# Optimization experiments

Hardware: AMD Instinct MI355X
Metric: run time of the kernel (lower is better)

The kernel has to match this reference:

```python
import jax, jax.numpy as jnp
import numpy as np

SIGMA_SPATIAL = 1.0
SIGMA_BILATERAL = 0.25
RADIUS = 1
PATCH = 2 * RADIUS + 1  # 3


def _spatial_kernel():
    x, y = np.mgrid[-RADIUS:RADIUS + 1, -RADIUS:RADIUS + 1]
    w1 = np.exp(-(x ** 2 + y ** 2) / (2.0 * SIGMA_SPATIAL ** 2))
    return jnp.asarray(w1.reshape(-1), dtype=jnp.float32)  # [PATCH*PATCH]


def _extract_patches(x):
    # x: [B,H,W,C] -> [B,H,W,PATCH*PATCH,C] via reflect-padded shifted slices
    B, H, W, C = x.shape
    xp = jnp.pad(x, ((0, 0), (RADIUS, RADIUS), (RADIUS, RADIUS), (0, 0)), mode='reflect')
    return jnp.stack(
        [xp[:, dy:dy + H, dx:dx + W, :] for dy in range(PATCH) for dx in range(PATCH)],
        axis=3,
    )


def setup_inputs() -> dict:
    key = jax.random.key(0)
    k1, k2 = jax.random.split(key)
    src = jax.random.uniform(k1, (2, 512, 512, 21), dtype=jnp.float32)
    im = jax.random.uniform(k2, (2, 512, 512, 3), dtype=jnp.float32)
    return {"src": src, "im": im}


def reference(src, im):
    w1 = _spatial_kernel()  # [9]
    im_patches = _extract_patches(im)                      # [B,H,W,9,Ci]
    diff2 = jnp.sum((im_patches - im[:, :, :, None, :]) ** 2, axis=-1)  # [B,H,W,9]
    w = jnp.exp(-diff2 / (2.0 * SIGMA_BILATERAL ** 2)) * w1            # [B,H,W,9]
    src_patches = _extract_patches(src)                    # [B,H,W,9,Cs]
    num = jnp.sum(src_patches * w[..., None], axis=3)      # [B,H,W,Cs]
    den = jnp.sum(w, axis=3, keepdims=True)                # [B,H,W,1]
    return num / den
```

## Files before the change

### kernel.cpp

```cpp
#include <hip/hip_runtime.h>

#define BATCH 2
#define H 512
#define W 512
#define CS 21
#define CI 3
#define P 128
#define R 8
#define TPB 384
#define GROWS (R + 2)
#define GSL (P + 2)
#define GSZ (GROWS * GSL * CI)

typedef float f32x4 __attribute__((ext_vector_type(4)));

__device__ __forceinline__ void fma4(float4& a, const float4 v, const float w) {
    a.x = fmaf(v.x, w, a.x);
    a.y = fmaf(v.y, w, a.y);
    a.z = fmaf(v.z, w, a.z);
    a.w = fmaf(v.w, w, a.w);
}

__device__ __forceinline__ void nt_store4(float* p, const float4 v) {
    __builtin_nontemporal_store(*(const f32x4*)&v, (f32x4*)p);
}

#define LOAD3(dst, rr, om, oc, op)                              \
    (dst)[0] = *(const float4*)(srow[rr] + (om));               \
    (dst)[1] = *(const float4*)(srow[rr] + (oc));               \
    (dst)[2] = *(const float4*)(srow[rr] + (op));

#define VA_I(r) ((r) < 6 ? (r) : 5)
#define VB_I(r) ((r) < 6 ? 0 : (r) - 6)
#define VR(va, vb, r, k) ((r) < 6 ? (va)[VA_I(r)][(k)] : (vb)[VB_I(r)][(k)])

#define COMPUTE8(va, vb, px, oc)                                             \
    {                                                                        \
        _Pragma("unroll")                                                    \
        for (int j = 0; j < R; ++j) {                                        \
            const float* wd = &s_w[((j << 7) + (px)) * 12];                  \
            float4 wA = *(const float4*)(wd + 0);                            \
            float4 wB = *(const float4*)(wd + 4);                            \
            float  w8 = wd[8];                                               \
            float4 acc = {0.f, 0.f, 0.f, 0.f};                               \
            fma4(acc, VR(va, vb, j + 0, 0), wA.x);                           \
            fma4(acc, VR(va, vb, j + 0, 1), wA.y);                           \
            fma4(acc, VR(va, vb, j + 0, 2), wA.z);                           \
            fma4(acc, VR(va, vb, j + 1, 0), wA.w);                           \
            fma4(acc, VR(va, vb, j + 1, 1), wB.x);                           \
            fma4(acc, VR(va, vb, j + 1, 2), wB.y);                           \
            fma4(acc, VR(va, vb, j + 2, 0), wB.z);                           \
            fma4(acc, VR(va, vb, j + 2, 1), wB.w);                           \
            fma4(acc, VR(va, vb, j + 2, 2), w8);                             \
            nt_store4(ob + (size_t)j * rs + (oc), acc);                      \
        }                                                                    \
    }

__global__ __launch_bounds__(TPB, 3) void jbu_kernel(
    const float* __restrict__ src, const float* __restrict__ im,
    float* __restrict__ out)
{
    __shared__ float s_g[GSZ];
    __shared__ __align__(16) float s_w[R * P * 12];

    const int t = threadIdx.x;

    const int f      = blockIdx.x;
    const int xcd    = f & 7;
    const int g      = f >> 3;
    const int rowgrp = (xcd << 3) | (g & 7);
    const int rem    = g >> 3;
    const int x0     = (rem & 3) << 7;
    const int b      = rem >> 2;
    const int y0     = rowgrp << 3;

    const size_t rs = (size_t)W * CS;
    const float* sb = src + (size_t)b * H * rs;
    const float* srow[GROWS];
    #pragma unroll
    for (int rr = 0; rr < GROWS; ++rr) {
        int v = y0 - 1 + rr;
        int tyr = (v < 0) ? 1 : ((v >= H) ? 2 * H - 2 - v : v);
        srow[rr] = sb + (size_t)tyr * rs + (size_t)x0 * CS;
    }

    const int px0   = t / 6;
    const int q0    = t - px0 * 6;
    const int coff0 = (q0 == 5) ? 17 : (q0 << 2);
    const int x_    = x0 + px0;
    const int xm_   = (x_ == 0)     ? 1     : x_ - 1;
    const int xp_   = (x_ == W - 1) ? W - 2 : x_ + 1;
    const int om0   = (xm_ - x0) * CS + coff0;
    const int oc0   = px0 * CS + coff0;
    const int op0   = (xp_ - x0) * CS + coff0;

    float4 va0[6][3];
    #pragma unroll
    for (int rr = 0; rr < 6; ++rr) { LOAD3(va0[rr], rr, om0, oc0, op0) }

    const float* imb = im + (size_t)b * (H * W * CI);
    for (int i = t; i < GSZ; i += TPB) {
        int rr   = i / (GSL * CI);
        int remi = i - rr * (GSL * CI);
        int slot = remi / CI;
        int ch   = remi - slot * CI;
        int gx   = x0 + slot - 1;
        gx = (gx < 0) ? 1 : ((gx >= W) ? W - 2 : gx);
        int vv = y0 - 1 + rr;
        int tyr = (vv < 0) ? 1 : ((vv >= H) ? 2 * H - 2 - vv : vv);
        const float* gsrc = imb + ((size_t)tyr * W + gx) * CI + ch;
        __builtin_amdgcn_global_load_lds(
            (const __attribute__((address_space(1))) void*)gsrc,
            (__attribute__((address_space(3))) void*)(s_g + i), 4, 0, 0);
    }
    __syncthreads();

    const int item1 = TPB + t;
    const int px1   = item1 / 6;
    const int q1    = item1 - px1 * 6;
    const int coff1 = (q1 == 5) ? 17 : (q1 << 2);
    const int x1    = x0 + px1;
    const int xm1   = (x1 == 0)     ? 1     : x1 - 1;
    const int xp1   = (x1 == W - 1) ? W - 2 : x1 + 1;
    const int om1   = (xm1 - x0) * CS + coff1;
    const int oc1   = px1 * CS + coff1;
    const int op1   = (xp1 - x0) * CS + coff1;

    float4 va1[6][3];
    #pragma unroll
    for (int rr = 0; rr < 4; ++rr) { LOAD3(va1[rr], rr, om1, oc1, op1) }

    {
        const float w1k[9] = {0.36787944f, 0.60653066f, 0.36787944f,
                              0.60653066f, 1.0f,        0.60653066f,
                              0.36787944f, 0.60653066f, 0.36787944f};
        #pragma unroll
        for (int ii = 0; ii < 3; ++ii) {
            int idx = ii * TPB + t;
            if (idx < R * P) {
                int r   = idx >> 7;
                int px  = idx & (P - 1);
                int cb  = ((r + 1) * GSL + px + 1) * CI;
                float c0 = s_g[cb + 0], c1 = s_g[cb + 1], c2 = s_g[cb + 2];
                float wv[9];
                float den = 0.f;
                #pragma unroll
                for (int k = 0; k < 9; ++k) {
                    int dy = k / 3, dx = k % 3;
                    int ib = ((r + dy) * GSL + px + dx) * CI;
                    float d0 = s_g[ib + 0] - c0;
                    float d1 = s_g[ib + 1] - c1;
                    float d2 = s_g[ib + 2] - c2;
                    float w = __expf(-8.0f * (d0 * d0 + d1 * d1 + d2 * d2)) * w1k[k];
                    wv[k] = w;
                    den += w;
                }
                float inv = 1.0f / den;
                float* wd = &s_w[idx * 12];
                *(float4*)(wd + 0) = make_float4(wv[0] * inv, wv[1] * inv, wv[2] * inv, wv[3] * inv);
                *(float4*)(wd + 4) = make_float4(wv[4] * inv, wv[5] * inv, wv[6] * inv, wv[7] * inv);
                wd[8] = wv[8] * inv;
            }
        }
    }
    __syncthreads();

    float* ob = out + ((size_t)(b * H + y0)) * rs + (size_t)x0 * CS;

    {
        float4 vb0[4][3];
        #pragma unroll
        for (int rr = 0; rr < 4; ++rr) { LOAD3(vb0[rr], rr + 6, om0, oc0, op0) }
        COMPUTE8(va0, vb0, px0, oc0)
    }

    {
        LOAD3(va1[4], 4, om1, oc1, op1)
        LOAD3(va1[5], 5, om1, oc1, op1)
        float4 vb1[4][3];
        #pragma unroll
        for (int rr = 0; rr < 4; ++rr) { LOAD3(vb1[rr], rr + 6, om1, oc1, op1) }
        COMPUTE8(va1, vb1, px1, oc1)
    }
}

extern "C" void kernel_launch(void* const* d_in, const int* in_sizes, int n_in,
                              void* d_out, int out_size, void* d_ws, size_t ws_size,
                              hipStream_t stream) {
    const float* src = (const float*)d_in[0];
    const float* im  = (const float*)d_in[1];
    float* out = (float*)d_out;
    dim3 grid((W / P) * (H / R) * BATCH, 1, 1);
    jbu_kernel<<<grid, TPB, 0, stream>>>(src, im, out);
}
```

Before: 106.3 us.

## Shrink tiles to 32 pixels, alias guide and weight LDS, one item per thread

Narrows each block's tile from 128 to 32 columns and halves threads per block, so every thread now handles one pixel/channel-group item instead of two. The guide-image buffer and the weight table now share one LDS array: weights are computed into registers, a barrier follows, and then they are written over the guide data. Grid size grows fourfold and LDS per block drops, which should allow more resident blocks and lower register pressure. In exchange, the 2-pixel halo is a larger fraction of each tile, so more redundant src and guide loads, and there is an extra barrier.

```diff
diff --git a/kernel.cpp b/kernel.cpp
--- a/kernel.cpp
+++ b/kernel.cpp
@@ -5,12 +5,14 @@
 #define W 512
 #define CS 21
 #define CI 3
-#define P 128
+#define P 32
 #define R 8
-#define TPB 384
+#define TPB 192
 #define GROWS (R + 2)
 #define GSL (P + 2)
 #define GSZ (GROWS * GSL * CI)
+#define NSETS (R * P)
+#define SWF (NSETS * 12)
 
 typedef float f32x4 __attribute__((ext_vector_type(4)));
 
@@ -38,7 +40,7 @@
     {                                                                        \
         _Pragma("unroll")                                                    \
         for (int j = 0; j < R; ++j) {                                        \
-            const float* wd = &s_w[((j << 7) + (px)) * 12];                  \
+            const float* wd = &s_u[((j * P) + (px)) * 12];                   \
             float4 wA = *(const float4*)(wd + 0);                            \
             float4 wB = *(const float4*)(wd + 4);                            \
             float  w8 = wd[8];                                               \
@@ -60,8 +62,7 @@
     const float* __restrict__ src, const float* __restrict__ im,
     float* __restrict__ out)
 {
-    __shared__ float s_g[GSZ];
-    __shared__ __align__(16) float s_w[R * P * 12];
+    __shared__ __align__(16) float s_u[SWF];
 
     const int t = threadIdx.x;
 
@@ -70,8 +71,8 @@
     const int g      = f >> 3;
     const int rowgrp = (xcd << 3) | (g & 7);
     const int rem    = g >> 3;
-    const int x0     = (rem & 3) << 7;
-    const int b      = rem >> 2;
+    const int x0     = (rem & 15) << 5;
+    const int b      = rem >> 4;
     const int y0     = rowgrp << 3;
 
     const size_t rs = (size_t)W * CS;
@@ -96,92 +97,83 @@
 
     float4 va0[6][3];
     #pragma unroll
-    for (int rr = 0; rr < 6; ++rr) { LOAD3(va0[rr], rr, om0, oc0, op0) }
+    for (int rr = 0; rr < 4; ++rr) { LOAD3(va0[rr], rr, om0, oc0, op0) }
 
     const float* imb = im + (size_t)b * (H * W * CI);
-    for (int i = t; i < GSZ; i += TPB) {
-        int rr   = i / (GSL * CI);
-        int remi = i - rr * (GSL * CI);
-        int slot = remi / CI;
-        int ch   = remi - slot * CI;
-        int gx   = x0 + slot - 1;
-        gx = (gx < 0) ? 1 : ((gx >= W) ? W - 2 : gx);
-        int vv = y0 - 1 + rr;
-        int tyr = (vv < 0) ? 1 : ((vv >= H) ? 2 * H - 2 - vv : vv);
-        const float* gsrc = imb + ((size_t)tyr * W + gx) * CI + ch;
-        __builtin_amdgcn_global_load_lds(
-            (const __attribute__((address_space(1))) void*)gsrc,
-            (__attribute__((address_space(3))) void*)(s_g + i), 4, 0, 0);
+    #pragma unroll
+    for (int ii = 0; ii < (GSZ + TPB - 1) / TPB; ++ii) {
+        int i = ii * TPB + t;
+        if (i < GSZ) {
+            int rr   = i / (GSL * CI);
+            int remi = i - rr * (GSL * CI);
+            int slot = remi / CI;
+            int ch   = remi - slot * CI;
+            int gx   = x0 + slot - 1;
+            gx = (gx < 0) ? 1 : ((gx >= W) ? W - 2 : gx);
+            int vv = y0 - 1 + rr;
+            int tyr = (vv < 0) ? 1 : ((vv >= H) ? 2 * H - 2 - vv : vv);
+            const float* gsrc = imb + ((size_t)tyr * W + gx) * CI + ch;
+            __builtin_amdgcn_global_load_lds(
+                (const __attribute__((address_space(1))) void*)gsrc,
+                (__attribute__((address_space(3))) void*)(s_u + i), 4, 0, 0);
+        }
     }
     __syncthreads();
 
-    const int item1 = TPB + t;
-    const int px1   = item1 / 6;
-    const int q1    = item1 - px1 * 6;
-    const int coff1 = (q1 == 5) ? 17 : (q1 << 2);
-    const int x1    = x0 + px1;
-    const int xm1   = (x1 == 0)     ? 1     : x1 - 1;
-    const int xp1   = (x1 == W - 1) ? W - 2 : x1 + 1;
-    const int om1   = (xm1 - x0) * CS + coff1;
-    const int oc1   = px1 * CS + coff1;
-    const int op1   = (xp1 - x0) * CS + coff1;
-
-    float4 va1[6][3];
-    #pragma unroll
-    for (int rr = 0; rr < 4; ++rr) { LOAD3(va1[rr], rr, om1, oc1, op1) }
-
+    float wreg[2][9];
     {
         const float w1k[9] = {0.36787944f, 0.60653066f, 0.36787944f,
                               0.60653066f, 1.0f,        0.60653066f,
                               0.36787944f, 0.60653066f, 0.36787944f};
         #pragma unroll
-        for (int ii = 0; ii < 3; ++ii) {
+        for (int ii = 0; ii < 2; ++ii) {
             int idx = ii * TPB + t;
-            if (idx < R * P) {
-                int r   = idx >> 7;
+            if (idx < NSETS) {
+                int r   = idx >> 5;
                 int px  = idx & (P - 1);
                 int cb  = ((r + 1) * GSL + px + 1) * CI;
-                float c0 = s_g[cb + 0], c1 = s_g[cb + 1], c2 = s_g[cb + 2];
+                float c0 = s_u[cb + 0], c1 = s_u[cb + 1], c2 = s_u[cb + 2];
                 float wv[9];
                 float den = 0.f;
                 #pragma unroll
                 for (int k = 0; k < 9; ++k) {
                     int dy = k / 3, dx = k % 3;
                     int ib = ((r + dy) * GSL + px + dx) * CI;
-                    float d0 = s_g[ib + 0] - c0;
-                    float d1 = s_g[ib + 1] - c1;
-                    float d2 = s_g[ib + 2] - c2;
+                    float d0 = s_u[ib + 0] - c0;
+                    float d1 = s_u[ib + 1] - c1;
+                    float d2 = s_u[ib + 2] - c2;
                     float w = __expf(-8.0f * (d0 * d0 + d1 * d1 + d2 * d2)) * w1k[k];
                     wv[k] = w;
                     den += w;
                 }
                 float inv = 1.0f / den;
-                float* wd = &s_w[idx * 12];
-                *(float4*)(wd + 0) = make_float4(wv[0] * inv, wv[1] * inv, wv[2] * inv, wv[3] * inv);
-                *(float4*)(wd + 4) = make_float4(wv[4] * inv, wv[5] * inv, wv[6] * inv, wv[7] * inv);
-                wd[8] = wv[8] * inv;
+                #pragma unroll
+                for (int k = 0; k < 9; ++k) wreg[ii][k] = wv[k] * inv;
             }
+        }
+    }
+    __syncthreads();
+
+    #pragma unroll
+    for (int ii = 0; ii < 2; ++ii) {
+        int idx = ii * TPB + t;
+        if (idx < NSETS) {
+            float* wd = &s_u[idx * 12];
+            *(float4*)(wd + 0) = make_float4(wreg[ii][0], wreg[ii][1], wreg[ii][2], wreg[ii][3]);
+            *(float4*)(wd + 4) = make_float4(wreg[ii][4], wreg[ii][5], wreg[ii][6], wreg[ii][7]);
+            wd[8] = wreg[ii][8];
         }
     }
     __syncthreads();
 
     float* ob = out + ((size_t)(b * H + y0)) * rs + (size_t)x0 * CS;
 
-    {
-        float4 vb0[4][3];
-        #pragma unroll
-        for (int rr = 0; rr < 4; ++rr) { LOAD3(vb0[rr], rr + 6, om0, oc0, op0) }
-        COMPUTE8(va0, vb0, px0, oc0)
-    }
-
-    {
-        LOAD3(va1[4], 4, om1, oc1, op1)
-        LOAD3(va1[5], 5, om1, oc1, op1)
-        float4 vb1[4][3];
-        #pragma unroll
-        for (int rr = 0; rr < 4; ++rr) { LOAD3(vb1[rr], rr + 6, om1, oc1, op1) }
-        COMPUTE8(va1, vb1, px1, oc1)
-    }
+    LOAD3(va0[4], 4, om0, oc0, op0)
+    LOAD3(va0[5], 5, om0, oc0, op0)
+    float4 vb0[4][3];
+    #pragma unroll
+    for (int rr = 0; rr < 4; ++rr) { LOAD3(vb0[rr], rr + 6, om0, oc0, op0) }
+    COMPUTE8(va0, vb0, px0, oc0)
 }
 
 extern "C" void kernel_launch(void* const* d_in, const int* in_sizes, int n_in,
```

Measured after the change: 102.8 us. 3.3% less time.
